# Optimization experiments

Measured on AMD Instinct MI355X. Metric: run time of the kernel, lower is better.

## Reference

```python
import jax, jax.numpy as jnp
import numpy as np

EMBED = 1024
HEADS = 16
HEAD_DIM = EMBED // HEADS


def setup_inputs() -> dict:
    key = jax.random.key(0)
    ks = jax.random.split(key, 6)
    N, S = 4, 1024
    query = jax.random.normal(ks[0], (N, S, EMBED), dtype=jnp.float32)
    keys = jax.random.normal(ks[1], (N, S, EMBED), dtype=jnp.float32)
    values = jax.random.normal(ks[2], (N, S, EMBED), dtype=jnp.float32)
    mask = jax.random.randint(ks[3], (N, 1, S, S), 0, 2, dtype=jnp.int32)
    W_out = jax.random.normal(ks[4], (EMBED, EMBED), dtype=jnp.float32) * (1.0 / np.sqrt(EMBED))
    b_out = jax.random.normal(ks[5], (EMBED,), dtype=jnp.float32) * 0.02
    return {"query": query, "keys": keys, "values": values, "mask": mask,
            "W_out": W_out, "b_out": b_out}


def reference(query, keys, values, mask, W_out, b_out):
    N, Q, _ = query.shape
    K = keys.shape[1]
    # NOTE: the torch module never applies its per-head q/k/v Linear layers;
    # only the reshape + attention + fc_out are in the forward path.
    q = query.reshape(N, Q, HEADS, HEAD_DIM)
    k = keys.reshape(N, K, HEADS, HEAD_DIM)
    v = values.reshape(N, K, HEADS, HEAD_DIM)
    # energy: [N, H, Q, K]
    energy = jnp.einsum("bqhd,bkhd->bhqk", q, k)
    energy = jnp.where(mask == 0, jnp.float32(-1e20), energy)
    attn = jax.nn.softmax(energy / jnp.sqrt(jnp.float32(HEAD_DIM)), axis=3)
    out = jnp.einsum("bhqk,bkhd->bqhd", attn, v).reshape(N, Q, HEADS * HEAD_DIM)
    return out @ W_out.T + b_out
```

## Files before the change

kernel.cpp:

```cpp
#include <hip/hip_runtime.h>
#include <math.h>

#define NB 4
#define SL 1024
#define EMB 1024
#define NH 16
#define HD 64
#define QB 128

typedef __attribute__((ext_vector_type(8))) short bf16x8;
typedef __attribute__((ext_vector_type(4))) float f32x4;
typedef __attribute__((ext_vector_type(4))) unsigned u32x4;

static __device__ __forceinline__ unsigned pk2(float a, float b) {
    unsigned x = __float_as_uint(a) + 0x8000u;
    unsigned y = __float_as_uint(b) + 0x8000u;
    return (x >> 16) | (y & 0xFFFF0000u);
}
static __device__ __forceinline__ float exp2_fast(float x) {
    float r; asm("v_exp_f32 %0, %1" : "=v"(r) : "v"(x)); return r;
}
static __device__ __forceinline__ unsigned cvtpk(float a, float b) {
    unsigned r; asm("v_cvt_pk_bf16_f32 %0, %1, %2" : "=v"(r) : "v"(a), "v"(b)); return r;
}
static __device__ __forceinline__ void gload_lds16(const void* g, void* l) {
    __builtin_amdgcn_global_load_lds(
        (const __attribute__((address_space(1))) unsigned int*)g,
        (__attribute__((address_space(3))) unsigned int*)l, 16, 0, 0);
}

#define VMW(n) asm volatile("s_waitcnt vmcnt(" #n ")" ::: "memory")
#define MEMPIN() asm volatile("" ::: "memory")

__global__ __launch_bounds__(256) void prep(
    const float* __restrict__ W, unsigned short* __restrict__ Wb,
    const float* __restrict__ Kf, unsigned short* __restrict__ Kb,
    const float* __restrict__ V, unsigned short* __restrict__ Vt,
    const int* __restrict__ mask, unsigned long long* __restrict__ Mbt)
{
    __shared__ unsigned short sT[128 * 68];
    const int bid = blockIdx.x, tid = threadIdx.x;
    const float CSC = 0.125f * 1.44269504f;

    if (bid < 512) {
        int i = (bid * 256 + tid) * 8;
        float4 f0 = *(const float4*)&W[i];
        float4 f1 = *(const float4*)&W[i + 4];
        uint4 u = { pk2(f0.x,f0.y), pk2(f0.z,f0.w), pk2(f1.x,f1.y), pk2(f1.z,f1.w) };
        *(uint4*)&Wb[i] = u;
    } else if (bid < 2560) {
        int t = bid - 512;
        int b = t >> 9, h = (t >> 5) & 15, k0 = (t & 31) * 32;
        int r = tid >> 3, d = (tid & 7) * 8;
        const float* gp = &Kf[((size_t)(b * SL + k0 + r)) * EMB + h * HD + d];
        float4 f0 = *(const float4*)gp, f1 = *(const float4*)(gp + 4);
        uint4 u = { pk2(f0.x*CSC,f0.y*CSC), pk2(f0.z*CSC,f0.w*CSC),
                    pk2(f1.x*CSC,f1.y*CSC), pk2(f1.z*CSC,f1.w*CSC) };
        *(uint4*)&Kb[((size_t)((b * NH + h) * SL + k0 + r)) * HD + d] = u;
    } else if (bid < 3072) {
        int t = bid - 2560;
        int bh = t >> 3, kb = t & 7;
        int b = bh >> 4, h = bh & 15;
        int k0 = kb * 128;
        #pragma unroll
        for (int i = 0; i < 4; ++i) {
            int lin = (i * 256 + tid) * 8;
            int r = lin >> 6, d = lin & 63;
            const float* gp = &V[((size_t)(b * SL + k0 + r)) * EMB + h * HD + d];
            float4 f0 = *(const float4*)gp, f1 = *(const float4*)(gp + 4);
            uint2 u0 = { pk2(f0.x,f0.y), pk2(f0.z,f0.w) };
            uint2 u1 = { pk2(f1.x,f1.y), pk2(f1.z,f1.w) };
            *(uint2*)&sT[r * 68 + d]     = u0;
            *(uint2*)&sT[r * 68 + d + 4] = u1;
        }
        __syncthreads();
        #pragma unroll
        for (int p = 0; p < 4; ++p) {
            int d = p * 16 + (tid >> 4);
            int c = tid & 15;
            unsigned v[4];
            #pragma unroll
            for (int j = 0; j < 4; ++j) {
                unsigned lo = sT[(c * 8 + 2 * j) * 68 + d];
                unsigned hi = sT[(c * 8 + 2 * j + 1) * 68 + d];
                v[j] = lo | (hi << 16);
            }
            uint4 u = { v[0], v[1], v[2], v[3] };
            *(uint4*)&Vt[((size_t)(bh * HD + d)) * SL + k0 + c * 8] = u;
        }
    } else {
        int t = bid - 3072;
        int lane = tid & 63;
        #pragma unroll
        for (int r = 0; r < 4; ++r) {
            int wid = (t * 4 + (tid >> 6)) * 4 + r;
            int c = wid & 15, q = (wid >> 4) & 1023, bb = wid >> 14;
            int mv = mask[((size_t)bb * SL + q) * SL + c * 64 + lane];
            unsigned long long bits = __ballot(mv != 0);
            if (lane == 0) Mbt[((size_t)bb * 16 + c) * SL + q] = bits;
        }
    }
}

__global__ __launch_bounds__(512, 4) void attn_mfma(
    const float* __restrict__ Q, const unsigned short* __restrict__ Kb,
    const unsigned short* __restrict__ Vt,
    const unsigned long long* __restrict__ Mbt,
    unsigned short* __restrict__ Oa)
{
    const int lin = blockIdx.x;
    const int xcd = lin & 7, slot = lin >> 3;
    const int bh = xcd * 8 + (slot >> 3);
    const int q0 = (slot & 7) * QB;
    const int b = bh >> 4, h = bh & 15;
    const int tid = threadIdx.x;
    const int w = tid >> 6, lane = tid & 63;
    const int m16 = lane & 15, quad = lane >> 4;
    const int lr = lane >> 3, lc = lane & 7;
    const int grp = w >> 2;
    const int wq = w & 3;
    const int srow = w * 8;

    __shared__ __align__(16) unsigned short sAll[32768];
    unsigned short* sKb = sAll;
    unsigned short* sVb = sAll + 16384;

    const size_t vbase = (size_t)(bh * HD) * SL;
    const size_t kbase = (size_t)(bh * SL) * HD;
    const unsigned long long* Mp = Mbt + (size_t)(b * 16) * SL + q0 + wq * 32 + m16;

    float4 qf[2][4];
    #pragma unroll
    for (int u = 0; u < 2; ++u) {
        const float* qp = &Q[((size_t)(b * SL + q0 + wq * 32 + u * 16 + m16)) * EMB + h * HD + quad * 8];
        qf[u][0] = *(const float4*)qp;        qf[u][1] = *(const float4*)(qp + 4);
        qf[u][2] = *(const float4*)(qp + 32); qf[u][3] = *(const float4*)(qp + 36);
    }
    MEMPIN();
    #pragma unroll
    for (int t2 = 0; t2 < 2; ++t2) {
        gload_lds16(&Vt[vbase + (size_t)(srow + lr) * SL + t2 * 64 + (lc ^ lr) * 8],
                    &sVb[t2 * 4096 + srow * 64]);
        gload_lds16(&Kb[kbase + (size_t)(t2 * 64 + srow + lr) * HD + (lc ^ lr) * 8],
                    &sKb[t2 * 4096 + srow * 64]);
    }
    MEMPIN();
    unsigned long long mbC0 = Mp[(size_t)grp * SL];
    unsigned long long mbC1 = Mp[(size_t)grp * SL + 16];
    unsigned long long mbN0 = 0, mbN1 = 0;
    MEMPIN();

    bf16x8 bQ[2][2];
    #pragma unroll
    for (int u = 0; u < 2; ++u) {
        u32x4 u0 = { pk2(qf[u][0].x,qf[u][0].y), pk2(qf[u][0].z,qf[u][0].w),
                     pk2(qf[u][1].x,qf[u][1].y), pk2(qf[u][1].z,qf[u][1].w) };
        u32x4 u1 = { pk2(qf[u][2].x,qf[u][2].y), pk2(qf[u][2].z,qf[u][2].w),
                     pk2(qf[u][3].x,qf[u][3].y), pk2(qf[u][3].z,qf[u][3].w) };
        bQ[u][0] = __builtin_bit_cast(bf16x8, u0);
        bQ[u][1] = __builtin_bit_cast(bf16x8, u1);
    }

    f32x4 O[2][4] = {};
    f32x4 lacc[2] = {};
    const short one_bf = (short)0x3F80;
    const bf16x8 ones = { one_bf, one_bf, one_bf, one_bf, one_bf, one_bf, one_bf, one_bf };

    for (int i = 0; i < 8; ++i) {
        VMW(2);
        __builtin_amdgcn_s_barrier();
        __builtin_amdgcn_sched_barrier(0);

        const int t = 2 * i + grp;
        if (i < 7) {
            const int tE = 2 * i + 2;
            const int bE = tE & 3, bO = (tE + 1) & 3;
            gload_lds16(&Vt[vbase + (size_t)(srow + lr) * SL + tE * 64 + (lc ^ lr) * 8],
                        &sVb[bE * 4096 + srow * 64]);
            gload_lds16(&Kb[kbase + (size_t)(tE * 64 + srow + lr) * HD + (lc ^ lr) * 8],
                        &sKb[bE * 4096 + srow * 64]);
            gload_lds16(&Vt[vbase + (size_t)(srow + lr) * SL + (tE + 1) * 64 + (lc ^ lr) * 8],
                        &sVb[bO * 4096 + srow * 64]);
            gload_lds16(&Kb[kbase + (size_t)((tE + 1) * 64 + srow + lr) * HD + (lc ^ lr) * 8],
                        &sKb[bO * 4096 + srow * 64]);
            MEMPIN();
            mbN0 = Mp[(size_t)(t + 2) * SL];
            mbN1 = Mp[(size_t)(t + 2) * SL + 16];
            MEMPIN();
        }

        const unsigned short* kc = &sKb[(t & 3) * 4096];
        const unsigned short* vc = &sVb[(t & 3) * 4096];

        f32x4 sc[2][4];
        __builtin_amdgcn_s_setprio(1);
        #pragma unroll
        for (int t4 = 0; t4 < 4; ++t4) {
            int krow = t4 * 16 + m16;
            bf16x8 a0 = *(const bf16x8*)&kc[krow * 64 + ((quad ^ (krow & 7)) * 8)];
            bf16x8 a1 = *(const bf16x8*)&kc[krow * 64 + (((4 + quad) ^ (krow & 7)) * 8)];
            f32x4 z = {0.f, 0.f, 0.f, 0.f};
            sc[0][t4] = __builtin_amdgcn_mfma_f32_16x16x32_bf16(a0, bQ[0][0], z,         0,0,0);
            sc[0][t4] = __builtin_amdgcn_mfma_f32_16x16x32_bf16(a1, bQ[0][1], sc[0][t4], 0,0,0);
            sc[1][t4] = __builtin_amdgcn_mfma_f32_16x16x32_bf16(a0, bQ[1][0], z,         0,0,0);
            sc[1][t4] = __builtin_amdgcn_mfma_f32_16x16x32_bf16(a1, bQ[1][1], sc[1][t4], 0,0,0);
        }
        __builtin_amdgcn_s_setprio(0);

        bf16x8 bP[2][2];
        #pragma unroll
        for (int u = 0; u < 2; ++u) {
            unsigned long long mb = u ? mbC1 : mbC0;
            unsigned s0 = ((unsigned)mb) >> (quad * 8);
            unsigned s1 = ((unsigned)(mb >> 32)) >> (quad * 8);
            unsigned wt[4][2];
            #pragma unroll
            for (int t4 = 0; t4 < 4; ++t4) {
                wt[t4][0] = cvtpk(exp2_fast(sc[u][t4][0]), exp2_fast(sc[u][t4][1]));
                wt[t4][1] = cvtpk(exp2_fast(sc[u][t4][2]), exp2_fast(sc[u][t4][3]));
            }
            unsigned g[2][4];
            #pragma unroll
            for (int hh = 0; hh < 2; ++hh)
                #pragma unroll
                for (int p = 0; p < 2; ++p) {
                    unsigned A = wt[2 * hh][p], B = wt[2 * hh + 1][p];
                    asm("v_permlane32_swap_b32 %0, %1" : "+v"(A), "+v"(B));
                    asm("v_permlane16_swap_b32 %0, %1" : "+v"(A), "+v"(B));
                    g[hh][p] = A; g[hh][2 + p] = B;
                }
            #pragma unroll
            for (int hh = 0; hh < 2; ++hh) {
                unsigned sb = hh ? s1 : s0;
                #pragma unroll
                for (int j2 = 0; j2 < 4; ++j2) {
                    unsigned mlo = (unsigned)(((int)(sb << (31 - 2 * j2))) >> 31);
                    unsigned mhi = (unsigned)(((int)(sb << (30 - 2 * j2))) >> 31);
                    g[hh][j2] &= (mlo & 0xFFFFu) | (mhi & 0xFFFF0000u);
                }
            }
            u32x4 p0 = { g[0][0], g[0][1], g[0][2], g[0][3] };
            u32x4 p1 = { g[1][0], g[1][1], g[1][2], g[1][3] };
            bP[u][0] = __builtin_bit_cast(bf16x8, p0);
            bP[u][1] = __builtin_bit_cast(bf16x8, p1);
        }

        __builtin_amdgcn_s_setprio(1);
        lacc[0] = __builtin_amdgcn_mfma_f32_16x16x32_bf16(ones, bP[0][0], lacc[0], 0,0,0);
        lacc[0] = __builtin_amdgcn_mfma_f32_16x16x32_bf16(ones, bP[0][1], lacc[0], 0,0,0);
        lacc[1] = __builtin_amdgcn_mfma_f32_16x16x32_bf16(ones, bP[1][0], lacc[1], 0,0,0);
        lacc[1] = __builtin_amdgcn_mfma_f32_16x16x32_bf16(ones, bP[1][1], lacc[1], 0,0,0);

        #pragma unroll
        for (int dt = 0; dt < 4; ++dt) {
            int drow = dt * 16 + m16;
            bf16x8 v0 = *(const bf16x8*)&vc[drow * 64 + ((quad ^ (drow & 7)) * 8)];
            bf16x8 v1 = *(const bf16x8*)&vc[drow * 64 + (((4 + quad) ^ (drow & 7)) * 8)];
            O[0][dt] = __builtin_amdgcn_mfma_f32_16x16x32_bf16(v0, bP[0][0], O[0][dt], 0,0,0);
            O[0][dt] = __builtin_amdgcn_mfma_f32_16x16x32_bf16(v1, bP[0][1], O[0][dt], 0,0,0);
            O[1][dt] = __builtin_amdgcn_mfma_f32_16x16x32_bf16(v0, bP[1][0], O[1][dt], 0,0,0);
            O[1][dt] = __builtin_amdgcn_mfma_f32_16x16x32_bf16(v1, bP[1][1], O[1][dt], 0,0,0);
        }
        __builtin_amdgcn_s_setprio(0);

        mbC0 = mbN0; mbC1 = mbN1;
    }

    __syncthreads();
    float* sM = (float*)sAll;
    if (grp == 1) {
        #pragma unroll
        for (int u = 0; u < 2; ++u)
            #pragma unroll
            for (int dt = 0; dt < 4; ++dt)
                *(f32x4*)&sM[((u * 4 + dt) * 256 + wq * 64 + lane) * 4] = O[u][dt];
        sM[8192 + (wq * 64 + lane) * 2 + 0] = lacc[0][0];
        sM[8192 + (wq * 64 + lane) * 2 + 1] = lacc[1][0];
    }
    __syncthreads();
    if (grp == 0) {
        float l[2];
        l[0] = lacc[0][0] + sM[8192 + (wq * 64 + lane) * 2 + 0];
        l[1] = lacc[1][0] + sM[8192 + (wq * 64 + lane) * 2 + 1];
        #pragma unroll
        for (int u = 0; u < 2; ++u) {
            float inv = 1.f / l[u];
            size_t base = ((size_t)(b * SL + q0 + wq * 32 + u * 16 + m16)) * EMB + h * HD + quad * 4;
            #pragma unroll
            for (int dt = 0; dt < 4; ++dt) {
                f32x4 part = *(const f32x4*)&sM[((u * 4 + dt) * 256 + wq * 64 + lane) * 4];
                f32x4 o = O[u][dt] + part;
                uint2 ow = { cvtpk(o[0] * inv, o[1] * inv),
                             cvtpk(o[2] * inv, o[3] * inv) };
                *(uint2*)&Oa[base + dt * 16] = ow;
            }
        }
    }
}

__global__ __launch_bounds__(256, 2) void proj_mfma(
    const unsigned short* __restrict__ A, const unsigned short* __restrict__ Wb,
    const float* __restrict__ bias, float* __restrict__ C)
{
    const int lin = blockIdx.x;
    const int xcd = lin & 7, idx = lin >> 3;
    const int m0 = (xcd * 4 + (idx >> 4)) * 128;
    const int n0 = (idx & 15) * 64;
    const int tid = threadIdx.x;
    const int w = tid >> 6, lane = tid & 63;
    const int m16 = lane & 15, quad = lane >> 4;
    const int lr = lane >> 3, lc = lane & 7;
    const int wm = (w >> 1) * 64, wn = (w & 1) * 32;

    __shared__ __align__(16) unsigned short sA[3][128 * 64];
    __shared__ __align__(16) unsigned short sW[3][64 * 64];

    f32x4 acc[4][2] = {};

    #define PSTAGE(IT, BI)                                                        \
    {                                                                             \
        const int e0_ = (IT) * 64;                                                \
        _Pragma("unroll")                                                         \
        for (int i_ = 0; i_ < 4; ++i_) {                                          \
            int r_ = w * 32 + i_ * 8;                                             \
            gload_lds16(&A[(size_t)(m0 + r_ + lr) * EMB + e0_ + (lc ^ lr) * 8],   \
                        &sA[BI][r_ * 64]);                                        \
        }                                                                         \
        _Pragma("unroll")                                                         \
        for (int i_ = 0; i_ < 2; ++i_) {                                          \
            int r_ = w * 16 + i_ * 8;                                             \
            gload_lds16(&Wb[(size_t)(n0 + r_ + lr) * EMB + e0_ + (lc ^ lr) * 8],  \
                        &sW[BI][r_ * 64]);                                        \
        }                                                                         \
    }

    PSTAGE(0, 0)
    MEMPIN();
    PSTAGE(1, 1)
    MEMPIN();

    for (int it = 0; it < 16; ++it) {
        if (it < 15) { VMW(6); } else { VMW(0); }
        __builtin_amdgcn_s_barrier();
        __builtin_amdgcn_sched_barrier(0);

        if (it < 14) {
            const int bn = (it + 2) % 3;
            PSTAGE(it + 2, bn)
            MEMPIN();
        }

        const int bf = it % 3;
        #pragma unroll
        for (int hh = 0; hh < 2; ++hh) {
            bf16x8 af[4], bw[2];
            #pragma unroll
            for (int mt = 0; mt < 4; ++mt) {
                int r = wm + mt * 16 + m16;
                af[mt] = *(const bf16x8*)&sA[bf][r * 64 + (((hh * 4 + quad) ^ (r & 7)) * 8)];
            }
            #pragma unroll
            for (int nt = 0; nt < 2; ++nt) {
                int r = wn + nt * 16 + m16;
                bw[nt] = *(const bf16x8*)&sW[bf][r * 64 + (((hh * 4 + quad) ^ (r & 7)) * 8)];
            }
            #pragma unroll
            for (int mt = 0; mt < 4; ++mt)
                #pragma unroll
                for (int nt = 0; nt < 2; ++nt)
                    acc[mt][nt] = __builtin_amdgcn_mfma_f32_16x16x32_bf16(af[mt], bw[nt], acc[mt][nt], 0,0,0);
        }
    }

    #pragma unroll
    for (int nt = 0; nt < 2; ++nt) {
        float bv = bias[n0 + wn + nt * 16 + m16];
        #pragma unroll
        for (int mt = 0; mt < 4; ++mt) {
            size_t row = (size_t)(m0 + wm + mt * 16 + quad * 4);
            #pragma unroll
            for (int rg = 0; rg < 4; ++rg)
                C[(row + rg) * EMB + n0 + wn + nt * 16 + m16] = acc[mt][nt][rg] + bv;
        }
    }
}

extern "C" void kernel_launch(void* const* d_in, const int* in_sizes, int n_in,
                              void* d_out, int out_size, void* d_ws, size_t ws_size,
                              hipStream_t stream) {
    const float* Q    = (const float*)d_in[0];
    const float* K    = (const float*)d_in[1];
    const float* V    = (const float*)d_in[2];
    const int*   mask = (const int*)  d_in[3];
    const float* W    = (const float*)d_in[4];
    const float* bias = (const float*)d_in[5];

    unsigned short* Oa = (unsigned short*)d_ws;
    unsigned short* Wb = Oa + (size_t)NB * SL * EMB;
    unsigned long long* Mbt = (unsigned long long*)(Wb + (size_t)EMB * EMB);
    unsigned short* Vt = (unsigned short*)(Mbt + (size_t)NB * 16 * SL);
    unsigned short* Kb = Vt + (size_t)NB * NH * HD * SL;

    prep<<<7168, 256, 0, stream>>>(W, Wb, K, Kb, V, Vt, mask, Mbt);
    attn_mfma<<<512, 512, 0, stream>>>(Q, Kb, Vt, Mbt, Oa);
    proj_mfma<<<512, 256, 0, stream>>>(Oa, Wb, bias, (float*)d_out);
}
```

Before: 151.1 us.

## Load V fragments directly from global memory instead of staging through LDS

The V tiles are no longer copied into shared memory. Each wave now reads its MFMA operand fragments for V straight from global (L2) memory, issued early in each iteration so the loads overlap with the QK^T and softmax work. This shrinks LDS from 64KB to about 34KB, which may allow more blocks per CU, and removes the V async copies and LDS reads. The cost is that the four waves sharing a tile each fetch V redundantly from global memory, and global latency is exposed if the loads are not hidden. The end-of-loop reduction scratch still fits in the smaller LDS buffer.

New measurement: 183.4 us. 21.4% more time.

```diff
diff --git a/kernel.cpp b/kernel.cpp
--- a/kernel.cpp
+++ b/kernel.cpp
@@ -121,13 +121,13 @@
     const int wq = w & 3;
     const int srow = w * 8;
 
-    __shared__ __align__(16) unsigned short sAll[32768];
+    __shared__ __align__(16) unsigned short sAll[17408];
     unsigned short* sKb = sAll;
-    unsigned short* sVb = sAll + 16384;
 
     const size_t vbase = (size_t)(bh * HD) * SL;
     const size_t kbase = (size_t)(bh * SL) * HD;
     const unsigned long long* Mp = Mbt + (size_t)(b * 16) * SL + q0 + wq * 32 + m16;
+    const unsigned short* Vp = Vt + vbase;
 
     float4 qf[2][4];
     #pragma unroll
@@ -137,13 +137,8 @@
         qf[u][2] = *(const float4*)(qp + 32); qf[u][3] = *(const float4*)(qp + 36);
     }
     MEMPIN();
-    #pragma unroll
-    for (int t2 = 0; t2 < 2; ++t2) {
-        gload_lds16(&Vt[vbase + (size_t)(srow + lr) * SL + t2 * 64 + (lc ^ lr) * 8],
-                    &sVb[t2 * 4096 + srow * 64]);
-        gload_lds16(&Kb[kbase + (size_t)(t2 * 64 + srow + lr) * HD + (lc ^ lr) * 8],
-                    &sKb[t2 * 4096 + srow * 64]);
-    }
+    gload_lds16(&Kb[kbase + (size_t)(srow + lr) * HD + (lc ^ lr) * 8],      &sKb[srow * 64]);
+    gload_lds16(&Kb[kbase + (size_t)(64 + srow + lr) * HD + (lc ^ lr) * 8], &sKb[4096 + srow * 64]);
     MEMPIN();
     unsigned long long mbC0 = Mp[(size_t)grp * SL];
     unsigned long long mbC1 = Mp[(size_t)grp * SL + 16];
@@ -172,17 +167,20 @@
         __builtin_amdgcn_sched_barrier(0);
 
         const int t = 2 * i + grp;
+        const unsigned short* vp = Vp + t * 64;
+
+        bf16x8 vf0 = *(const bf16x8*)&vp[(size_t)(m16) * SL + quad * 8];
+        bf16x8 vf1 = *(const bf16x8*)&vp[(size_t)(m16) * SL + (4 + quad) * 8];
+        bf16x8 vf2 = *(const bf16x8*)&vp[(size_t)(16 + m16) * SL + quad * 8];
+        bf16x8 vf3 = *(const bf16x8*)&vp[(size_t)(16 + m16) * SL + (4 + quad) * 8];
+        MEMPIN();
+
         if (i < 7) {
             const int tE = 2 * i + 2;
-            const int bE = tE & 3, bO = (tE + 1) & 3;
-            gload_lds16(&Vt[vbase + (size_t)(srow + lr) * SL + tE * 64 + (lc ^ lr) * 8],
-                        &sVb[bE * 4096 + srow * 64]);
             gload_lds16(&Kb[kbase + (size_t)(tE * 64 + srow + lr) * HD + (lc ^ lr) * 8],
-                        &sKb[bE * 4096 + srow * 64]);
-            gload_lds16(&Vt[vbase + (size_t)(srow + lr) * SL + (tE + 1) * 64 + (lc ^ lr) * 8],
-                        &sVb[bO * 4096 + srow * 64]);
+                        &sKb[(tE & 3) * 4096 + srow * 64]);
             gload_lds16(&Kb[kbase + (size_t)((tE + 1) * 64 + srow + lr) * HD + (lc ^ lr) * 8],
-                        &sKb[bO * 4096 + srow * 64]);
+                        &sKb[((tE + 1) & 3) * 4096 + srow * 64]);
             MEMPIN();
             mbN0 = Mp[(size_t)(t + 2) * SL];
             mbN1 = Mp[(size_t)(t + 2) * SL + 16];
@@ -190,7 +188,6 @@
         }
 
         const unsigned short* kc = &sKb[(t & 3) * 4096];
-        const unsigned short* vc = &sVb[(t & 3) * 4096];
 
         f32x4 sc[2][4];
         __builtin_amdgcn_s_setprio(1);
@@ -245,22 +242,34 @@
             bP[u][1] = __builtin_bit_cast(bf16x8, p1);
         }
 
+        bf16x8 vg0 = *(const bf16x8*)&vp[(size_t)(32 + m16) * SL + quad * 8];
+        bf16x8 vg1 = *(const bf16x8*)&vp[(size_t)(32 + m16) * SL + (4 + quad) * 8];
+        bf16x8 vg2 = *(const bf16x8*)&vp[(size_t)(48 + m16) * SL + quad * 8];
+        bf16x8 vg3 = *(const bf16x8*)&vp[(size_t)(48 + m16) * SL + (4 + quad) * 8];
+        MEMPIN();
+
         __builtin_amdgcn_s_setprio(1);
         lacc[0] = __builtin_amdgcn_mfma_f32_16x16x32_bf16(ones, bP[0][0], lacc[0], 0,0,0);
         lacc[0] = __builtin_amdgcn_mfma_f32_16x16x32_bf16(ones, bP[0][1], lacc[0], 0,0,0);
         lacc[1] = __builtin_amdgcn_mfma_f32_16x16x32_bf16(ones, bP[1][0], lacc[1], 0,0,0);
         lacc[1] = __builtin_amdgcn_mfma_f32_16x16x32_bf16(ones, bP[1][1], lacc[1], 0,0,0);
 
-        #pragma unroll
-        for (int dt = 0; dt < 4; ++dt) {
-            int drow = dt * 16 + m16;
-            bf16x8 v0 = *(const bf16x8*)&vc[drow * 64 + ((quad ^ (drow & 7)) * 8)];
-            bf16x8 v1 = *(const bf16x8*)&vc[drow * 64 + (((4 + quad) ^ (drow & 7)) * 8)];
-            O[0][dt] = __builtin_amdgcn_mfma_f32_16x16x32_bf16(v0, bP[0][0], O[0][dt], 0,0,0);
-            O[0][dt] = __builtin_amdgcn_mfma_f32_16x16x32_bf16(v1, bP[0][1], O[0][dt], 0,0,0);
-            O[1][dt] = __builtin_amdgcn_mfma_f32_16x16x32_bf16(v0, bP[1][0], O[1][dt], 0,0,0);
-            O[1][dt] = __builtin_amdgcn_mfma_f32_16x16x32_bf16(v1, bP[1][1], O[1][dt], 0,0,0);
-        }
+        O[0][0] = __builtin_amdgcn_mfma_f32_16x16x32_bf16(vf0, bP[0][0], O[0][0], 0,0,0);
+        O[0][0] = __builtin_amdgcn_mfma_f32_16x16x32_bf16(vf1, bP[0][1], O[0][0], 0,0,0);
+        O[1][0] = __builtin_amdgcn_mfma_f32_16x16x32_bf16(vf0, bP[1][0], O[1][0], 0,0,0);
+        O[1][0] = __builtin_amdgcn_mfma_f32_16x16x32_bf16(vf1, bP[1][1], O[1][0], 0,0,0);
+        O[0][1] = __builtin_amdgcn_mfma_f32_16x16x32_bf16(vf2, bP[0][0], O[0][1], 0,0,0);
+        O[0][1] = __builtin_amdgcn_mfma_f32_16x16x32_bf16(vf3, bP[0][1], O[0][1], 0,0,0);
+        O[1][1] = __builtin_amdgcn_mfma_f32_16x16x32_bf16(vf2, bP[1][0], O[1][1], 0,0,0);
+        O[1][1] = __builtin_amdgcn_mfma_f32_16x16x32_bf16(vf3, bP[1][1], O[1][1], 0,0,0);
+        O[0][2] = __builtin_amdgcn_mfma_f32_16x16x32_bf16(vg0, bP[0][0], O[0][2], 0,0,0);
+        O[0][2] = __builtin_amdgcn_mfma_f32_16x16x32_bf16(vg1, bP[0][1], O[0][2], 0,0,0);
+        O[1][2] = __builtin_amdgcn_mfma_f32_16x16x32_bf16(vg0, bP[1][0], O[1][2], 0,0,0);
+        O[1][2] = __builtin_amdgcn_mfma_f32_16x16x32_bf16(vg1, bP[1][1], O[1][2], 0,0,0);
+        O[0][3] = __builtin_amdgcn_mfma_f32_16x16x32_bf16(vg2, bP[0][0], O[0][3], 0,0,0);
+        O[0][3] = __builtin_amdgcn_mfma_f32_16x16x32_bf16(vg3, bP[0][1], O[0][3], 0,0,0);
+        O[1][3] = __builtin_amdgcn_mfma_f32_16x16x32_bf16(vg2, bP[1][0], O[1][3], 0,0,0);
+        O[1][3] = __builtin_amdgcn_mfma_f32_16x16x32_bf16(vg3, bP[1][1], O[1][3], 0,0,0);
         __builtin_amdgcn_s_setprio(0);
 
         mbC0 = mbN0; mbC1 = mbN1;
```
